# Kernel tuning notes

Hardware: AMD Instinct MI355X
Metric: run time of the kernel (lower is better)

The kernel has to match this reference:

```python
import jax, jax.numpy as jnp
import numpy as np

N_NODES = 50000
N_EDGES = 800000
F_IN = 128   # in_feats
H = 256      # h_feats
C = 32       # num_classes
E_IN = 2     # raw edge feature dim
EPS = 1e-12  # F.normalize eps


def _lin_params(key, fan_in, fan_out):
    kw, kb = jax.random.split(key)
    bound = 1.0 / np.sqrt(fan_in)
    W = jax.random.uniform(kw, (fan_in, fan_out), jnp.float32, -bound, bound)
    b = jax.random.uniform(kb, (fan_out,), jnp.float32, -bound, bound)
    return W, b


def setup_inputs() -> dict:
    key = jax.random.key(0)
    ks = jax.random.split(key, 12)
    inp = {
        "node_feat": jax.random.normal(ks[0], (N_NODES, F_IN), jnp.float32),
        "edge_feat": jax.random.normal(ks[1], (N_EDGES, E_IN), jnp.float32),
        "src": jax.random.randint(ks[2], (N_EDGES,), 0, N_NODES, jnp.int32),
        "dst": jax.random.randint(ks[3], (N_EDGES,), 0, N_NODES, jnp.int32),
    }
    # conv1: SAGEConv(F_IN, H, 2, F_IN)
    inp["We1"], inp["be1"] = _lin_params(ks[4], E_IN, F_IN)        # e_linear
    inp["Wr1a"], inp["br1a"] = _lin_params(ks[5], F_IN, F_IN)      # reduce_linear1
    inp["Wr1b"], inp["br1b"] = _lin_params(ks[6], F_IN, F_IN)      # reduce_linear2
    inp["Wl1"], inp["bl1"] = _lin_params(ks[7], 2 * F_IN, H)       # linear1
    # conv2: SAGEConv(H, C, F_IN, H)
    inp["We2"], inp["be2"] = _lin_params(ks[8], F_IN, H)
    inp["Wr2a"], inp["br2a"] = _lin_params(ks[9], H, H)
    inp["Wr2b"], inp["br2b"] = _lin_params(ks[10], H, H)
    inp["Wl2"], inp["bl2"] = _lin_params(ks[11], 2 * H, C)
    return inp


def _sage_conv(h, e, src, dst, We, be, Wra, bra, Wrb, brb, Wl, bl):
    # edge weight transform
    w = e @ We + be                                    # [E, e_out]
    hs = h[src]                                        # [E, F] gather
    hd = h[dst]
    # per-edge cosine similarity (scalar per edge)
    sn = hs / jnp.maximum(jnp.linalg.norm(hs, axis=1, keepdims=True), EPS)
    dn = hd / jnp.maximum(jnp.linalg.norm(hd, axis=1, keepdims=True), EPS)
    cos = jnp.sum(sn * dn, axis=1, keepdims=True)      # [E, 1]
    m = cos * w * hs                                   # message [E, F]
    # mailbox MLP applied per-edge, then mean-reduce per dst node
    r = jax.nn.relu(m @ Wra + bra)
    r = jax.nn.relu(r @ Wrb + brb)
    s = jax.ops.segment_sum(r, dst, num_segments=N_NODES)
    cnt = jax.ops.segment_sum(jnp.ones((dst.shape[0], 1), r.dtype), dst,
                              num_segments=N_NODES)
    h_N = s / jnp.maximum(cnt, 1.0)                    # zero-degree nodes -> 0
    h_out = jnp.concatenate([h, h_N], axis=1) @ Wl + bl
    return h_out, w


def reference(node_feat, edge_feat, src, dst,
              We1, be1, Wr1a, br1a, Wr1b, br1b, Wl1, bl1,
              We2, be2, Wr2a, br2a, Wr2b, br2b, Wl2, bl2):
    h, e_h = _sage_conv(node_feat, edge_feat, src, dst,
                        We1, be1, Wr1a, br1a, Wr1b, br1b, Wl1, bl1)
    h, e_h = jax.nn.relu(h), jax.nn.relu(e_h)
    h, _ = _sage_conv(h, e_h, src, dst,
                      We2, be2, Wr2a, br2a, Wr2b, br2b, Wl2, bl2)
    return h  # [N_NODES, C] logits
```

## Files before the change

### kernel.cpp

```cpp
#include <hip/hip_runtime.h>
#include <math.h>

#define NN 50000
#define NE 800000
#define NWGE1 (NE / 128)
#define NWGE2 (NE / 128)

typedef short bf8 __attribute__((ext_vector_type(8)));
typedef short bf4v __attribute__((ext_vector_type(4)));
typedef short bf2v __attribute__((ext_vector_type(2)));
typedef float f4 __attribute__((ext_vector_type(4)));

__device__ __forceinline__ short f2b(float f) {
  unsigned int u = __float_as_uint(f);
  unsigned int r = (u + 0x7FFFu + ((u >> 16) & 1u)) >> 16;
  return (short)(unsigned short)r;
}
__device__ __forceinline__ float b2f(short s) {
  return __uint_as_float(((unsigned int)(unsigned short)s) << 16);
}
__device__ __forceinline__ f4 b2f4(bf4v p) {
  f4 v;
  v[0] = b2f(p[0]); v[1] = b2f(p[1]); v[2] = b2f(p[2]); v[3] = b2f(p[3]);
  return v;
}

__device__ __forceinline__ int swz8(int b, int nwg) {
  const int q = nwg >> 3, r = nwg & 7;
  const int x = b & 7, o = b >> 3;
  return (x < r ? x * (q + 1) : r * (q + 1) + (x - r) * q) + o;
}


__global__ __launch_bounds__(256) void prep_k(
    const float* __restrict__ Wr1a, const float* __restrict__ Wr1b,
    const float* __restrict__ We2,  const float* __restrict__ Wr2a,
    const float* __restrict__ Wr2b, const float* __restrict__ Wl1,
    short* __restrict__ WaT1, short* __restrict__ WbT1,
    short* __restrict__ We2T, short* __restrict__ WaT2,
    short* __restrict__ WbT2, short* __restrict__ Wl1T,
    const float* __restrict__ nf, short* __restrict__ nfb,
    const int* __restrict__ dst, int* __restrict__ cnt)
{
  const int b = blockIdx.x;
  if (b < 1024) {
    const float* in; short* out; int K, N, bb;
    if (b < 64)       { in = Wr1a; out = WaT1; K = 128; N = 128; bb = b; }
    else if (b < 128) { in = Wr1b; out = WbT1; K = 128; N = 128; bb = b - 64; }
    else if (b < 256) { in = We2;  out = We2T; K = 128; N = 256; bb = b - 128; }
    else if (b < 512) { in = Wr2a; out = WaT2; K = 256; N = 256; bb = b - 256; }
    else if (b < 768) { in = Wr2b; out = WbT2; K = 256; N = 256; bb = b - 512; }
    else              { in = Wl1;  out = Wl1T; K = 256; N = 256; bb = b - 768; }
    const int i = bb * 256 + threadIdx.x;
    if (i < K * N) {
      const int n = i / K, k = i - n * K;
      out[i] = f2b(in[(size_t)k * N + n]);
    }
  } else if (b < 7274) {
    const int i = (b - 1024) * 256 + threadIdx.x;
    f4 v = *(const f4*)&nf[(size_t)i * 4];
    bf4v p;
    p[0] = f2b(v[0]); p[1] = f2b(v[1]); p[2] = f2b(v[2]); p[3] = f2b(v[3]);
    *(bf4v*)&nfb[(size_t)i * 4] = p;
  } else {
    const int e = (b - 7274) * 256 + threadIdx.x;
    atomicAdd(&cnt[dst[e]], 1);
  }
}

__global__ __launch_bounds__(256) void norm1_k(const short* __restrict__ nfb,
                                               float* __restrict__ invn) {
  const int node = blockIdx.x * 4 + (threadIdx.x >> 6);
  if (node >= NN) return;
  const int lane = threadIdx.x & 63;
  bf2v hb = *(const bf2v*)&nfb[(size_t)node * 128 + lane * 2];
  float h0 = b2f(hb[0]), h1v = b2f(hb[1]);
  float ss = fmaf(h0, h0, h1v * h1v);
#pragma unroll
  for (int o = 32; o >= 1; o >>= 1) ss += __shfl_xor(ss, o);
  if (lane == 0) invn[node] = 1.f / fmaxf(sqrtf(ss), 1e-12f);
}

__global__ __launch_bounds__(256) void norm2_k(const short* __restrict__ h1b,
                                               float* __restrict__ invn) {
  const int node = blockIdx.x * 4 + (threadIdx.x >> 6);
  if (node >= NN) return;
  const int lane = threadIdx.x & 63;
  f4 h = b2f4(*(const bf4v*)&h1b[(size_t)node * 256 + lane * 4]);
  float ss = 0.f;
#pragma unroll
  for (int r = 0; r < 4; ++r) ss = fmaf(h[r], h[r], ss);
#pragma unroll
  for (int o = 32; o >= 1; o >>= 1) ss += __shfl_xor(ss, o);
  if (lane == 0) invn[node] = 1.f / fmaxf(sqrtf(ss), 1e-12f);
}


__global__ __launch_bounds__(1024) void scanA_k(const int* __restrict__ cnt,
                                                int* __restrict__ off2,
                                                int* __restrict__ bsum) {
  __shared__ int buf[1024];
  const int t = threadIdx.x;
  const int i = blockIdx.x * 1024 + t;
  const int v = (i < NN) ? cnt[i] : 0;
  buf[t] = v;
  __syncthreads();
#pragma unroll
  for (int o = 1; o < 1024; o <<= 1) {
    int x = (t >= o) ? buf[t - o] : 0;
    __syncthreads();
    buf[t] += x;
    __syncthreads();
  }
  if (i < NN) off2[i] = buf[t] - v;
  if (t == 1023) bsum[blockIdx.x] = buf[t];
}

__global__ __launch_bounds__(64) void scanB_k(int* __restrict__ bsum, int nb) {
  const int t = threadIdx.x;
  int v = (t < nb) ? bsum[t] : 0;
#pragma unroll
  for (int o = 1; o < 64; o <<= 1) {
    int x = __shfl_up(v, o);
    if (t >= o) v += x;
  }
  if (t < nb) bsum[t] = v;
}

__global__ __launch_bounds__(256) void scanC_k(int* __restrict__ off2,
                                               const int* __restrict__ bsum) {
  const int i = blockIdx.x * 256 + threadIdx.x;
  if (i >= NN) return;
  const int b = i >> 10;
  if (b) off2[i] += bsum[b - 1];
}

__global__ __launch_bounds__(256) void perm_k(const int* __restrict__ dst,
                                              int* __restrict__ off2,
                                              int* __restrict__ perm,
                                              int* __restrict__ dsts) {
  int e = blockIdx.x * 256 + threadIdx.x;
  if (e >= NE) return;
  int d = dst[e];
  int p = atomicAdd(&off2[d], 1);
  perm[p] = e;
  dsts[p] = d;
}


__global__ __launch_bounds__(512, 6) void edge_mlp1(
    const short* __restrict__ nfb, const float* __restrict__ ef,
    const int* __restrict__ src, const int* __restrict__ perm,
    const int* __restrict__ dsts, const float* __restrict__ invn1,
    const float* __restrict__ We1, const float* __restrict__ be1,
    const short* __restrict__ WaT, const float* __restrict__ ba,
    const short* __restrict__ WbT, const float* __restrict__ bbv,
    float* __restrict__ s1)
{
  __shared__ __align__(16) short Ms[128 * 136];
  __shared__ int dse[128];
  __shared__ int sse[128];
  __shared__ float2 efs[128];
  const int t = threadIdx.x;
  const int e0 = swz8(blockIdx.x, NWGE1) * 128;
  const int lane = t & 63, wv = t >> 6;

  if (t < 128) {
    const int pe = perm[e0 + t];
    dse[t] = dsts[e0 + t];
    sse[t] = src[pe];
    efs[t] = *(const float2*)&ef[2 * pe];
  }
  __syncthreads();

  {
    const int k2 = lane * 2;
    const float wA0 = We1[k2],       wA1 = We1[k2 + 1];
    const float wB0 = We1[128 + k2], wB1 = We1[128 + k2 + 1];
    const float bE0 = be1[k2],       bE1 = be1[k2 + 1];
#pragma unroll
    for (int ch = 0; ch < 2; ++ch) {
      bf2v hbv[8], dbv[8];
#pragma unroll
      for (int i = 0; i < 8; ++i) {
        const int e = wv * 16 + ch * 8 + i;
        hbv[i] = *(const bf2v*)&nfb[(size_t)sse[e] * 128 + k2];
        dbv[i] = *(const bf2v*)&nfb[(size_t)dse[e] * 128 + k2];
      }
#pragma unroll
      for (int i = 0; i < 8; ++i) {
        const int e = wv * 16 + ch * 8 + i;
        const int s = sse[e];
        const int d = dse[e];
        const float h0 = b2f(hbv[i][0]), h1v = b2f(hbv[i][1]);
        const float g0 = b2f(dbv[i][0]), g1 = b2f(dbv[i][1]);
        float sd = fmaf(h0, g0, h1v * g1);
#pragma unroll
        for (int o = 32; o >= 1; o >>= 1) sd += __shfl_xor(sd, o);
        const float c = sd * invn1[s] * invn1[d];
        const float2 f01 = efs[e];
        const float w0 = fmaf(f01.x, wA0, fmaf(f01.y, wB0, bE0));
        const float w1 = fmaf(f01.x, wA1, fmaf(f01.y, wB1, bE1));
        bf2v pk;
        pk[0] = f2b(c * w0 * h0);
        pk[1] = f2b(c * w1 * h1v);
        *(bf2v*)&Ms[e * 136 + k2] = pk;
      }
    }
  }
  __syncthreads();

  const int lr = lane & 15;
  const int lq = lane >> 4;
  const int n0 = wv * 16;

  f4 acc[8];
#pragma unroll
  for (int b = 0; b < 8; ++b) acc[b] = (f4)0.f;

#pragma unroll
  for (int kc = 0; kc < 128; kc += 32) {
    bf8 aF = *(const bf8*)&WaT[(size_t)(n0 + lr) * 128 + kc + lq * 8];
#pragma unroll
    for (int hf = 0; hf < 2; ++hf) {
      bf8 bF[4];
#pragma unroll
      for (int b2 = 0; b2 < 4; ++b2)
        bF[b2] = *(const bf8*)&Ms[((hf * 4 + b2) * 16 + lr) * 136 + kc + lq * 8];
      __builtin_amdgcn_s_setprio(1);
#pragma unroll
      for (int b2 = 0; b2 < 4; ++b2)
        acc[hf * 4 + b2] =
            __builtin_amdgcn_mfma_f32_16x16x32_bf16(aF, bF[b2], acc[hf * 4 + b2], 0, 0, 0);
      __builtin_amdgcn_s_setprio(0);
    }
  }
  __syncthreads();

  {
    const int n = n0 + lq * 4;
    f4 bb = *(const f4*)&ba[n];
#pragma unroll
    for (int b = 0; b < 8; ++b) {
      bf4v pk;
#pragma unroll
      for (int r = 0; r < 4; ++r) pk[r] = f2b(fmaxf(acc[b][r] + bb[r], 0.f));
      *(bf4v*)&Ms[(b * 16 + lr) * 136 + n] = pk;
    }
  }
  __syncthreads();

#pragma unroll
  for (int b = 0; b < 8; ++b) acc[b] = (f4)0.f;
#pragma unroll
  for (int kc = 0; kc < 128; kc += 32) {
    bf8 aF = *(const bf8*)&WbT[(size_t)(n0 + lr) * 128 + kc + lq * 8];
#pragma unroll
    for (int hf = 0; hf < 2; ++hf) {
      bf8 bF[4];
#pragma unroll
      for (int b2 = 0; b2 < 4; ++b2)
        bF[b2] = *(const bf8*)&Ms[((hf * 4 + b2) * 16 + lr) * 136 + kc + lq * 8];
      __builtin_amdgcn_s_setprio(1);
#pragma unroll
      for (int b2 = 0; b2 < 4; ++b2)
        acc[hf * 4 + b2] =
            __builtin_amdgcn_mfma_f32_16x16x32_bf16(aF, bF[b2], acc[hf * 4 + b2], 0, 0, 0);
      __builtin_amdgcn_s_setprio(0);
    }
  }
  __syncthreads();

  {
    const int n = n0 + lq * 4;
    f4 bb = *(const f4*)&bbv[n];
#pragma unroll
    for (int b = 0; b < 8; ++b) {
      bf4v pk;
#pragma unroll
      for (int r = 0; r < 4; ++r) pk[r] = f2b(fmaxf(acc[b][r] + bb[r], 0.f));
      *(bf4v*)&Ms[(b * 16 + lr) * 136 + n] = pk;
    }
  }
  __syncthreads();

  {
    const int f = t & 127;
    const int eb = (t >> 7) * 32;
    float run = 0.f;
    int pd = dse[eb];
#pragma unroll 4
    for (int e = eb; e < eb + 32; ++e) {
      const int d = dse[e];
      if (d != pd) {
        atomicAdd(&s1[(size_t)pd * 128 + f], run);
        run = 0.f;
        pd = d;
      }
      run += b2f(Ms[e * 136 + f]);
    }
    atomicAdd(&s1[(size_t)pd * 128 + f], run);
  }
}


__global__ __launch_bounds__(512, 4) void edge_mlp2(
    const short* __restrict__ h1b, const float* __restrict__ ef,
    const int* __restrict__ src, const int* __restrict__ perm,
    const int* __restrict__ dsts, const float* __restrict__ invn2,
    const float* __restrict__ We1, const float* __restrict__ be1,
    const short* __restrict__ We2T, const float* __restrict__ be2,
    const short* __restrict__ WaT, const float* __restrict__ ba,
    const short* __restrict__ WbT, const float* __restrict__ bbv,
    float* __restrict__ s2)
{
  __shared__ __align__(16) short U[128 * 264];
  __shared__ int dse[128];
  __shared__ int pes[128];
  __shared__ int sse[128];
  short* Ws  = U;
  short* M2s = U;
  const int t = threadIdx.x;
  const int e0 = swz8(blockIdx.x, NWGE2) * 128;
  const int lane = t & 63, wv = t >> 6;
  const int lr = lane & 15;
  const int lq = lane >> 4;
  const int n0 = wv * 32;

  if (t < 128) {
    const int pe = perm[e0 + t];
    pes[t] = pe;
    dse[t] = dsts[e0 + t];
    sse[t] = src[pe];
  }
  __syncthreads();

  {
    const int e = t >> 2;
    const int kb = (t & 3) * 32;
    const int pe = pes[e];
    const float f0 = ef[2 * pe], f1 = ef[2 * pe + 1];
#pragma unroll
    for (int j = 0; j < 4; ++j) {
      const int k = kb + j * 8;
      f4 wa0 = *(const f4*)&We1[k];
      f4 wa1 = *(const f4*)&We1[k + 4];
      f4 wb0 = *(const f4*)&We1[128 + k];
      f4 wb1 = *(const f4*)&We1[128 + k + 4];
      f4 b0 = *(const f4*)&be1[k];
      f4 b1 = *(const f4*)&be1[k + 4];
      bf8 pk;
#pragma unroll
      for (int x = 0; x < 4; ++x) {
        pk[x]     = f2b(fmaxf(fmaf(f0, wa0[x], fmaf(f1, wb0[x], b0[x])), 0.f));
        pk[x + 4] = f2b(fmaxf(fmaf(f0, wa1[x], fmaf(f1, wb1[x], b1[x])), 0.f));
      }
      *(bf8*)&Ws[e * 136 + k] = pk;
    }
  }
  __syncthreads();

  f4 acc[2][8];
#pragma unroll
  for (int a = 0; a < 2; ++a)
#pragma unroll
    for (int b = 0; b < 8; ++b) acc[a][b] = (f4)0.f;

#pragma unroll
  for (int kc = 0; kc < 128; kc += 32) {
    bf8 aF[2], bF[8];
#pragma unroll
    for (int a = 0; a < 2; ++a)
      aF[a] = *(const bf8*)&We2T[(size_t)(n0 + a * 16 + lr) * 128 + kc + lq * 8];
#pragma unroll
    for (int b = 0; b < 8; ++b)
      bF[b] = *(const bf8*)&Ws[(b * 16 + lr) * 136 + kc + lq * 8];
    __builtin_amdgcn_s_setprio(1);
#pragma unroll
    for (int a = 0; a < 2; ++a)
#pragma unroll
      for (int b = 0; b < 8; ++b)
        acc[a][b] = __builtin_amdgcn_mfma_f32_16x16x32_bf16(aF[a], bF[b], acc[a][b], 0, 0, 0);
    __builtin_amdgcn_s_setprio(0);
  }
  __syncthreads();

#pragma unroll
  for (int b = 0; b < 8; ++b) {
#pragma unroll
    for (int a = 0; a < 2; ++a) {
      const int n = n0 + a * 16 + lq * 4;
      f4 bb = *(const f4*)&be2[n];
      bf4v pk;
#pragma unroll
      for (int r = 0; r < 4; ++r) pk[r] = f2b(acc[a][b][r] + bb[r]);
      *(bf4v*)&M2s[(b * 16 + lr) * 264 + n] = pk;
    }
  }
  __syncthreads();

  {
    const int k4 = lane * 4;
#pragma unroll
    for (int ch = 0; ch < 2; ++ch) {
      bf4v hsv[8], hdv[8];
#pragma unroll
      for (int i = 0; i < 8; ++i) {
        const int e = wv * 16 + ch * 8 + i;
        hsv[i] = *(const bf4v*)&h1b[(size_t)sse[e] * 256 + k4];
        hdv[i] = *(const bf4v*)&h1b[(size_t)dse[e] * 256 + k4];
      }
#pragma unroll
      for (int i = 0; i < 8; ++i) {
        const int e = wv * 16 + ch * 8 + i;
        const int s = sse[e];
        const int d = dse[e];
        f4 hs = b2f4(hsv[i]);
        f4 hd = b2f4(hdv[i]);
        float sd = 0.f;
#pragma unroll
        for (int r = 0; r < 4; ++r) sd = fmaf(hs[r], hd[r], sd);
#pragma unroll
        for (int o = 32; o >= 1; o >>= 1) sd += __shfl_xor(sd, o);
        const float c = sd * invn2[s] * invn2[d];
        f4 w = b2f4(*(const bf4v*)&M2s[e * 264 + k4]);
        bf4v pk;
#pragma unroll
        for (int r = 0; r < 4; ++r) pk[r] = f2b(w[r] * c * hs[r]);
        *(bf4v*)&M2s[e * 264 + k4] = pk;
      }
    }
  }
  __syncthreads();

#pragma unroll
  for (int a = 0; a < 2; ++a)
#pragma unroll
    for (int b = 0; b < 8; ++b) acc[a][b] = (f4)0.f;
  for (int kc = 0; kc < 256; kc += 32) {
    bf8 aF[2], bF[8];
#pragma unroll
    for (int a = 0; a < 2; ++a)
      aF[a] = *(const bf8*)&WaT[(size_t)(n0 + a * 16 + lr) * 256 + kc + lq * 8];
#pragma unroll
    for (int b = 0; b < 8; ++b)
      bF[b] = *(const bf8*)&M2s[(b * 16 + lr) * 264 + kc + lq * 8];
    __builtin_amdgcn_s_setprio(1);
#pragma unroll
    for (int a = 0; a < 2; ++a)
#pragma unroll
      for (int b = 0; b < 8; ++b)
        acc[a][b] = __builtin_amdgcn_mfma_f32_16x16x32_bf16(aF[a], bF[b], acc[a][b], 0, 0, 0);
    __builtin_amdgcn_s_setprio(0);
  }
  __syncthreads();

#pragma unroll
  for (int a = 0; a < 2; ++a) {
    const int n = n0 + a * 16 + lq * 4;
    f4 bb = *(const f4*)&ba[n];
#pragma unroll
    for (int b = 0; b < 8; ++b) {
      bf4v pk;
#pragma unroll
      for (int r = 0; r < 4; ++r) pk[r] = f2b(fmaxf(acc[a][b][r] + bb[r], 0.f));
      *(bf4v*)&M2s[(b * 16 + lr) * 264 + n] = pk;
    }
  }
  __syncthreads();

#pragma unroll
  for (int a = 0; a < 2; ++a)
#pragma unroll
    for (int b = 0; b < 8; ++b) acc[a][b] = (f4)0.f;
  for (int kc = 0; kc < 256; kc += 32) {
    bf8 aF[2], bF[8];
#pragma unroll
    for (int a = 0; a < 2; ++a)
      aF[a] = *(const bf8*)&WbT[(size_t)(n0 + a * 16 + lr) * 256 + kc + lq * 8];
#pragma unroll
    for (int b = 0; b < 8; ++b)
      bF[b] = *(const bf8*)&M2s[(b * 16 + lr) * 264 + kc + lq * 8];
    __builtin_amdgcn_s_setprio(1);
#pragma unroll
    for (int a = 0; a < 2; ++a)
#pragma unroll
      for (int b = 0; b < 8; ++b)
        acc[a][b] = __builtin_amdgcn_mfma_f32_16x16x32_bf16(aF[a], bF[b], acc[a][b], 0, 0, 0);
    __builtin_amdgcn_s_setprio(0);
  }
  __syncthreads();

  float* RF = (float*)M2s;
#pragma unroll
  for (int h = 0; h < 2; ++h) {
    if ((wv >> 2) == h) {
#pragma unroll
      for (int a = 0; a < 2; ++a) {
        const int n = n0 + a * 16 + lq * 4;
        f4 bb = *(const f4*)&bbv[n];
#pragma unroll
        for (int b = 0; b < 8; ++b) {
          f4 v;
#pragma unroll
          for (int r = 0; r < 4; ++r) v[r] = fmaxf(acc[a][b][r] + bb[r], 0.f);
          *(f4*)&RF[(b * 16 + lr) * 132 + (n - h * 128)] = v;
        }
      }
    }
    __syncthreads();
    {
      const int f = t & 127;
      const int eb = (t >> 7) * 32;
      float run = 0.f;
      int pd = dse[eb];
#pragma unroll 4
      for (int e = eb; e < eb + 32; ++e) {
        const int d = dse[e];
        if (d != pd) {
          atomicAdd(&s2[(size_t)pd * 256 + h * 128 + f], run);
          run = 0.f;
          pd = d;
        }
        run += RF[e * 132 + f];
      }
      atomicAdd(&s2[(size_t)pd * 256 + h * 128 + f], run);
    }
    __syncthreads();
  }
}


__global__ __launch_bounds__(256, 3) void h1m_k(
    const float* __restrict__ nf, const float* __restrict__ s1,
    const int* __restrict__ cnt, const short* __restrict__ Wl1T,
    const float* __restrict__ bl1, short* __restrict__ h1b)
{
  __shared__ __align__(16) short As[64 * 264];
  const int t = threadIdx.x;
  const int v0 = blockIdx.x * 64;

  {
    const int row = t >> 2;
    const int kb = (t & 3) * 64;
    int gn = v0 + row;
    if (gn >= NN) gn = NN - 1;
    const float inv = 1.f / fmaxf((float)cnt[gn], 1.f);
#pragma unroll
    for (int j = 0; j < 64; j += 8) {
      const int k = kb + j;
      f4 x0, x1;
      if (k < 128) {
        x0 = *(const f4*)&nf[(size_t)gn * 128 + k];
        x1 = *(const f4*)&nf[(size_t)gn * 128 + k + 4];
      } else {
        x0 = *(const f4*)&s1[(size_t)gn * 128 + (k - 128)];
        x1 = *(const f4*)&s1[(size_t)gn * 128 + (k - 124)];
#pragma unroll
        for (int x = 0; x < 4; ++x) { x0[x] *= inv; x1[x] *= inv; }
      }
      bf8 pk;
#pragma unroll
      for (int x = 0; x < 4; ++x) { pk[x] = f2b(x0[x]); pk[x + 4] = f2b(x1[x]); }
      *(bf8*)&As[row * 264 + k] = pk;
    }
  }
  __syncthreads();

  const int lane = t & 63, wv = t >> 6;
  const int lr = lane & 15;
  const int lq = lane >> 4;
  const int n0 = wv * 64;

  f4 acc[4][4];
#pragma unroll
  for (int a = 0; a < 4; ++a)
#pragma unroll
    for (int b = 0; b < 4; ++b) acc[a][b] = (f4)0.f;

  for (int kc = 0; kc < 256; kc += 32) {
    bf8 aF[4], bF[4];
#pragma unroll
    for (int a = 0; a < 4; ++a)
      aF[a] = *(const bf8*)&Wl1T[(size_t)(n0 + a * 16 + lr) * 256 + kc + lq * 8];
#pragma unroll
    for (int b = 0; b < 4; ++b)
      bF[b] = *(const bf8*)&As[(b * 16 + lr) * 264 + kc + lq * 8];
#pragma unroll
    for (int a = 0; a < 4; ++a)
#pragma unroll
      for (int b = 0; b < 4; ++b)
        acc[a][b] = __builtin_amdgcn_mfma_f32_16x16x32_bf16(aF[a], bF[b], acc[a][b], 0, 0, 0);
  }

#pragma unroll
  for (int b = 0; b < 4; ++b) {
    const int gn = v0 + b * 16 + lr;
    if (gn >= NN) continue;
#pragma unroll
    for (int a = 0; a < 4; ++a) {
      const int n = n0 + a * 16 + lq * 4;
      f4 bb = *(const f4*)&bl1[n];
      bf4v pk;
      pk[0] = f2b(fmaxf(acc[a][b][0] + bb[0], 0.f));
      pk[1] = f2b(fmaxf(acc[a][b][1] + bb[1], 0.f));
      pk[2] = f2b(fmaxf(acc[a][b][2] + bb[2], 0.f));
      pk[3] = f2b(fmaxf(acc[a][b][3] + bb[3], 0.f));
      *(bf4v*)&h1b[(size_t)gn * 256 + n] = pk;
    }
  }
}


__global__ __launch_bounds__(256) void out_k(
    const short* __restrict__ h1b, const float* __restrict__ s2,
    const int* __restrict__ cnt, const float* __restrict__ Wl2,
    const float* __restrict__ bl2, float* __restrict__ out)
{
  __shared__ float A8[8][512];
  const int n0 = blockIdx.x * 8;
  const int tx = threadIdx.x;
  const int ty = threadIdx.y;
  const int t = ty * 32 + tx;
  const int row = t >> 5;
  const int k0 = (t & 31) * 16;
  const int n = n0 + row;
  const float inv = 1.0f / fmaxf((float)cnt[n], 1.0f);
#pragma unroll
  for (int i = 0; i < 16; i += 4) {
    int k = k0 + i;
    f4 v;
    if (k < 256) {
      v = b2f4(*(const bf4v*)&h1b[(size_t)n * 256 + k]);
    } else {
      v = *(const f4*)&s2[(size_t)n * 256 + (k - 256)];
      v[0] *= inv; v[1] *= inv; v[2] *= inv; v[3] *= inv;
    }
    *(f4*)&A8[row][k] = v;
  }
  __syncthreads();
  float acc = bl2[tx];
#pragma unroll 8
  for (int k = 0; k < 512; k++) acc = fmaf(A8[ty][k], Wl2[(size_t)k * 32 + tx], acc);
  out[(size_t)(n0 + ty) * 32 + tx] = acc;
}


extern "C" void kernel_launch(void* const* d_in, const int* in_sizes, int n_in,
                              void* d_out, int out_size, void* d_ws, size_t ws_size,
                              hipStream_t stream) {
  const float* nf   = (const float*)d_in[0];
  const float* ef   = (const float*)d_in[1];
  const int*   src  = (const int*)d_in[2];
  const int*   dst  = (const int*)d_in[3];
  const float* We1  = (const float*)d_in[4];
  const float* be1  = (const float*)d_in[5];
  const float* Wr1a = (const float*)d_in[6];
  const float* br1a = (const float*)d_in[7];
  const float* Wr1b = (const float*)d_in[8];
  const float* br1b = (const float*)d_in[9];
  const float* Wl1  = (const float*)d_in[10];
  const float* bl1  = (const float*)d_in[11];
  const float* We2  = (const float*)d_in[12];
  const float* be2  = (const float*)d_in[13];
  const float* Wr2a = (const float*)d_in[14];
  const float* br2a = (const float*)d_in[15];
  const float* Wr2b = (const float*)d_in[16];
  const float* br2b = (const float*)d_in[17];
  const float* Wl2  = (const float*)d_in[18];
  const float* bl2  = (const float*)d_in[19];

  float* ws = (float*)d_ws;
  float* s1   = ws;
  float* s2   = s1 + (size_t)NN * 128;
  int*   cnt  = (int*)(s2 + (size_t)NN * 256);
  short* h1b  = (short*)(cnt + NN);
  short* nfb  = h1b + (size_t)NN * 256;
  short* WaT1 = nfb + (size_t)NN * 128;
  short* WbT1 = WaT1 + 128 * 128;
  short* We2T = WbT1 + 128 * 128;
  short* WaT2 = We2T + 256 * 128;
  short* WbT2 = WaT2 + 256 * 256;
  short* Wl1T = WbT2 + 256 * 256;
  int*   off2 = (int*)(Wl1T + 256 * 256);
  int*   perm = off2 + NN;
  int*   dsts = perm + NE;
  float* invn1 = (float*)(dsts + NE);
  float* invn2 = invn1 + NN;
  int*   bsum  = (int*)(invn2 + NN);

  size_t need = ((size_t)NN * 128 + (size_t)NN * 256 + NN) * 4 +
                ((size_t)NN * 256 + (size_t)NN * 128 +
                 (size_t)128 * 128 * 2 + (size_t)256 * 128 +
                 (size_t)256 * 256 * 3) * 2 +
                ((size_t)NN + 2 * (size_t)NE + 2 * (size_t)NN) * 4 + 64 * 4;
  if (ws_size < need) return;

  hipMemsetAsync(s1, 0, ((size_t)NN * 128 + (size_t)NN * 256 + NN) * 4, stream);

  prep_k<<<10399, 256, 0, stream>>>(Wr1a, Wr1b, We2, Wr2a, Wr2b, Wl1,
                                    WaT1, WbT1, We2T, WaT2, WbT2, Wl1T,
                                    nf, nfb, dst, cnt);
  norm1_k<<<(NN + 3) / 4, 256, 0, stream>>>(nfb, invn1);

  const int nb = (NN + 1023) / 1024;
  scanA_k<<<nb, 1024, 0, stream>>>(cnt, off2, bsum);
  scanB_k<<<1, 64, 0, stream>>>(bsum, nb);
  scanC_k<<<(NN + 255) / 256, 256, 0, stream>>>(off2, bsum);
  perm_k<<<NE / 256, 256, 0, stream>>>(dst, off2, perm, dsts);

  edge_mlp1<<<NWGE1, 512, 0, stream>>>(nfb, ef, src, perm, dsts, invn1,
                                       We1, be1, WaT1, br1a, WbT1, br1b, s1);

  h1m_k<<<(NN + 63) / 64, 256, 0, stream>>>(nf, s1, cnt, Wl1T, bl1, h1b);
  norm2_k<<<(NN + 3) / 4, 256, 0, stream>>>(h1b, invn2);

  edge_mlp2<<<NWGE2, 512, 0, stream>>>(h1b, ef, src, perm, dsts, invn2,
                                       We1, be1, We2T, be2, WaT2, br2a,
                                       WbT2, br2b, s2);

  out_k<<<NN / 8, dim3(32, 8), 0, stream>>>(h1b, s2, cnt, Wl2, bl2, (float*)d_out);
}
```

Before: 1.089 ms.

## Double edge tile per workgroup in edge_mlp2 to 256 edges

```diff
diff --git a/kernel.cpp b/kernel.cpp
--- a/kernel.cpp
+++ b/kernel.cpp
@@ -4,7 +4,7 @@
 #define NN 50000
 #define NE 800000
 #define NWGE1 (NE / 128)
-#define NWGE2 (NE / 128)
+#define NWGE2 (NE / 256)
 
 typedef short bf8 __attribute__((ext_vector_type(8)));
 typedef short bf4v __attribute__((ext_vector_type(4)));
@@ -304,7 +304,7 @@
 }
 
 
-__global__ __launch_bounds__(512, 4) void edge_mlp2(
+__global__ __launch_bounds__(512, 2) void edge_mlp2(
     const short* __restrict__ h1b, const float* __restrict__ ef,
     const int* __restrict__ src, const int* __restrict__ perm,
     const int* __restrict__ dsts, const float* __restrict__ invn2,
@@ -314,20 +314,20 @@
     const short* __restrict__ WbT, const float* __restrict__ bbv,
     float* __restrict__ s2)
 {
-  __shared__ __align__(16) short U[128 * 264];
-  __shared__ int dse[128];
-  __shared__ int pes[128];
-  __shared__ int sse[128];
+  __shared__ __align__(16) short U[256 * 264];
+  __shared__ int dse[256];
+  __shared__ int pes[256];
+  __shared__ int sse[256];
   short* Ws  = U;
   short* M2s = U;
   const int t = threadIdx.x;
-  const int e0 = swz8(blockIdx.x, NWGE2) * 128;
+  const int e0 = swz8(blockIdx.x, NWGE2) * 256;
   const int lane = t & 63, wv = t >> 6;
   const int lr = lane & 15;
   const int lq = lane >> 4;
   const int n0 = wv * 32;
 
-  if (t < 128) {
+  if (t < 256) {
     const int pe = perm[e0 + t];
     pes[t] = pe;
     dse[t] = dsts[e0 + t];
@@ -336,12 +336,12 @@
   __syncthreads();
 
   {
-    const int e = t >> 2;
-    const int kb = (t & 3) * 32;
+    const int e = t >> 1;
+    const int kb = (t & 1) * 64;
     const int pe = pes[e];
     const float f0 = ef[2 * pe], f1 = ef[2 * pe + 1];
 #pragma unroll
-    for (int j = 0; j < 4; ++j) {
+    for (int j = 0; j < 8; ++j) {
       const int k = kb + j * 8;
       f4 wa0 = *(const f4*)&We1[k];
       f4 wa1 = *(const f4*)&We1[k + 4];
@@ -360,33 +360,38 @@
   }
   __syncthreads();
 
-  f4 acc[2][8];
+  f4 acc[2][16];
 #pragma unroll
   for (int a = 0; a < 2; ++a)
 #pragma unroll
-    for (int b = 0; b < 8; ++b) acc[a][b] = (f4)0.f;
+    for (int b = 0; b < 16; ++b) acc[a][b] = (f4)0.f;
 
 #pragma unroll
   for (int kc = 0; kc < 128; kc += 32) {
-    bf8 aF[2], bF[8];
+    bf8 aF[2];
 #pragma unroll
     for (int a = 0; a < 2; ++a)
       aF[a] = *(const bf8*)&We2T[(size_t)(n0 + a * 16 + lr) * 128 + kc + lq * 8];
 #pragma unroll
-    for (int b = 0; b < 8; ++b)
-      bF[b] = *(const bf8*)&Ws[(b * 16 + lr) * 136 + kc + lq * 8];
-    __builtin_amdgcn_s_setprio(1);
-#pragma unroll
-    for (int a = 0; a < 2; ++a)
-#pragma unroll
-      for (int b = 0; b < 8; ++b)
-        acc[a][b] = __builtin_amdgcn_mfma_f32_16x16x32_bf16(aF[a], bF[b], acc[a][b], 0, 0, 0);
-    __builtin_amdgcn_s_setprio(0);
-  }
-  __syncthreads();
-
-#pragma unroll
-  for (int b = 0; b < 8; ++b) {
+    for (int hf = 0; hf < 2; ++hf) {
+      bf8 bF[8];
+#pragma unroll
+      for (int b2 = 0; b2 < 8; ++b2)
+        bF[b2] = *(const bf8*)&Ws[((hf * 8 + b2) * 16 + lr) * 136 + kc + lq * 8];
+      __builtin_amdgcn_s_setprio(1);
+#pragma unroll
+      for (int a = 0; a < 2; ++a)
+#pragma unroll
+        for (int b2 = 0; b2 < 8; ++b2)
+          acc[a][hf * 8 + b2] = __builtin_amdgcn_mfma_f32_16x16x32_bf16(
+              aF[a], bF[b2], acc[a][hf * 8 + b2], 0, 0, 0);
+      __builtin_amdgcn_s_setprio(0);
+    }
+  }
+  __syncthreads();
+
+#pragma unroll
+  for (int b = 0; b < 16; ++b) {
 #pragma unroll
     for (int a = 0; a < 2; ++a) {
       const int n = n0 + a * 16 + lq * 4;
@@ -402,17 +407,17 @@
   {
     const int k4 = lane * 4;
 #pragma unroll
-    for (int ch = 0; ch < 2; ++ch) {
+    for (int ch = 0; ch < 4; ++ch) {
       bf4v hsv[8], hdv[8];
 #pragma unroll
       for (int i = 0; i < 8; ++i) {
-        const int e = wv * 16 + ch * 8 + i;
+        const int e = wv * 32 + ch * 8 + i;
         hsv[i] = *(const bf4v*)&h1b[(size_t)sse[e] * 256 + k4];
         hdv[i] = *(const bf4v*)&h1b[(size_t)dse[e] * 256 + k4];
       }
 #pragma unroll
       for (int i = 0; i < 8; ++i) {
-        const int e = wv * 16 + ch * 8 + i;
+        const int e = wv * 32 + ch * 8 + i;
         const int s = sse[e];
         const int d = dse[e];
         f4 hs = b2f4(hsv[i]);
@@ -436,22 +441,27 @@
 #pragma unroll
   for (int a = 0; a < 2; ++a)
 #pragma unroll
-    for (int b = 0; b < 8; ++b) acc[a][b] = (f4)0.f;
+    for (int b = 0; b < 16; ++b) acc[a][b] = (f4)0.f;
   for (int kc = 0; kc < 256; kc += 32) {
-    bf8 aF[2], bF[8];
+    bf8 aF[2];
 #pragma unroll
     for (int a = 0; a < 2; ++a)
       aF[a] = *(const bf8*)&WaT[(size_t)(n0 + a * 16 + lr) * 256 + kc + lq * 8];
 #pragma unroll
-    for (int b = 0; b < 8; ++b)
-      bF[b] = *(const bf8*)&M2s[(b * 16 + lr) * 264 + kc + lq * 8];
-    __builtin_amdgcn_s_setprio(1);
-#pragma unroll
-    for (int a = 0; a < 2; ++a)
-#pragma unroll
-      for (int b = 0; b < 8; ++b)
-        acc[a][b] = __builtin_amdgcn_mfma_f32_16x16x32_bf16(aF[a], bF[b], acc[a][b], 0, 0, 0);
-    __builtin_amdgcn_s_setprio(0);
+    for (int hf = 0; hf < 2; ++hf) {
+      bf8 bF[8];
+#pragma unroll
+      for (int b2 = 0; b2 < 8; ++b2)
+        bF[b2] = *(const bf8*)&M2s[((hf * 8 + b2) * 16 + lr) * 264 + kc + lq * 8];
+      __builtin_amdgcn_s_setprio(1);
+#pragma unroll
+      for (int a = 0; a < 2; ++a)
+#pragma unroll
+        for (int b2 = 0; b2 < 8; ++b2)
+          acc[a][hf * 8 + b2] = __builtin_amdgcn_mfma_f32_16x16x32_bf16(
+              aF[a], bF[b2], acc[a][hf * 8 + b2], 0, 0, 0);
+      __builtin_amdgcn_s_setprio(0);
+    }
   }
   __syncthreads();
 
@@ -460,7 +470,7 @@
     const int n = n0 + a * 16 + lq * 4;
     f4 bb = *(const f4*)&ba[n];
 #pragma unroll
-    for (int b = 0; b < 8; ++b) {
+    for (int b = 0; b < 16; ++b) {
       bf4v pk;
 #pragma unroll
       for (int r = 0; r < 4; ++r) pk[r] = f2b(fmaxf(acc[a][b][r] + bb[r], 0.f));
@@ -472,22 +482,27 @@
 #pragma unroll
   for (int a = 0; a < 2; ++a)
 #pragma unroll
-    for (int b = 0; b < 8; ++b) acc[a][b] = (f4)0.f;
+    for (int b = 0; b < 16; ++b) acc[a][b] = (f4)0.f;
   for (int kc = 0; kc < 256; kc += 32) {
-    bf8 aF[2], bF[8];
+    bf8 aF[2];
 #pragma unroll
     for (int a = 0; a < 2; ++a)
       aF[a] = *(const bf8*)&WbT[(size_t)(n0 + a * 16 + lr) * 256 + kc + lq * 8];
 #pragma unroll
-    for (int b = 0; b < 8; ++b)
-      bF[b] = *(const bf8*)&M2s[(b * 16 + lr) * 264 + kc + lq * 8];
-    __builtin_amdgcn_s_setprio(1);
-#pragma unroll
-    for (int a = 0; a < 2; ++a)
-#pragma unroll
-      for (int b = 0; b < 8; ++b)
-        acc[a][b] = __builtin_amdgcn_mfma_f32_16x16x32_bf16(aF[a], bF[b], acc[a][b], 0, 0, 0);
-    __builtin_amdgcn_s_setprio(0);
+    for (int hf = 0; hf < 2; ++hf) {
+      bf8 bF[8];
+#pragma unroll
+      for (int b2 = 0; b2 < 8; ++b2)
+        bF[b2] = *(const bf8*)&M2s[((hf * 8 + b2) * 16 + lr) * 264 + kc + lq * 8];
+      __builtin_amdgcn_s_setprio(1);
+#pragma unroll
+      for (int a = 0; a < 2; ++a)
+#pragma unroll
+        for (int b2 = 0; b2 < 8; ++b2)
+          acc[a][hf * 8 + b2] = __builtin_amdgcn_mfma_f32_16x16x32_bf16(
+              aF[a], bF[b2], acc[a][hf * 8 + b2], 0, 0, 0);
+      __builtin_amdgcn_s_setprio(0);
+    }
   }
   __syncthreads();
 
@@ -500,7 +515,7 @@
         const int n = n0 + a * 16 + lq * 4;
         f4 bb = *(const f4*)&bbv[n];
 #pragma unroll
-        for (int b = 0; b < 8; ++b) {
+        for (int b = 0; b < 16; ++b) {
           f4 v;
 #pragma unroll
           for (int r = 0; r < 4; ++r) v[r] = fmaxf(acc[a][b][r] + bb[r], 0.f);
@@ -511,11 +526,11 @@
     __syncthreads();
     {
       const int f = t & 127;
-      const int eb = (t >> 7) * 32;
+      const int eb = (t >> 7) * 64;
       float run = 0.f;
       int pd = dse[eb];
 #pragma unroll 4
-      for (int e = eb; e < eb + 32; ++e) {
+      for (int e = eb; e < eb + 64; ++e) {
         const int d = dse[e];
         if (d != pd) {
           atomicAdd(&s2[(size_t)pd * 256 + h * 128 + f], run);
```

Result: slower. 1.112 ms (+2.2%).
